# Kernel optimization log

Hardware: AMD Instinct MI355X
Metric: run time of the kernel (lower is better)

Reference implementation:

```python
import jax, jax.numpy as jnp
import numpy as np

B, N, T = 256, 512, 96
E, H, K = 8, 128, 2
PROB_THRESHOLD = 0.05
# SG auto-anneal: first forward sets temperature = t_max = 10.0 (cosine decay at step 0)
TEMP = 10.0


def setup_inputs() -> dict:
    key = jax.random.key(0)
    ks = jax.random.split(key, 8)
    s_g = 1.0 / np.sqrt(T)
    s_1 = 1.0 / np.sqrt(T)
    s_2 = 1.0 / np.sqrt(H)
    return {
        "x": jax.random.normal(ks[0], (B, N, T), dtype=jnp.float32),
        "Wg": jax.random.uniform(ks[1], (E, T), jnp.float32, -s_g, s_g),   # gate Linear(T, E)
        "bg": jax.random.uniform(ks[2], (E,), jnp.float32, -s_g, s_g),
        "W1": jax.random.uniform(ks[3], (E, T, H), jnp.float32, -s_1, s_1),  # stacked MLPExpert fc1
        "b1": jax.random.uniform(ks[4], (E, H), jnp.float32, -s_1, s_1),
        "W2": jax.random.uniform(ks[5], (E, H, T), jnp.float32, -s_2, s_2),  # stacked MLPExpert fc2
        "b2": jax.random.uniform(ks[6], (E, T), jnp.float32, -s_2, s_2),
        "route_scale": jnp.asarray(1.2, dtype=jnp.float32),
    }


def reference(x, Wg, bg, W1, b1, W2, b2, route_scale):
    b, n, t = x.shape
    BN = b * n
    xf = x.reshape(BN, t)                              # [BN, T]

    # ---- SG gate (eval mode: no noise; temp = t_max after first anneal step) ----
    logits = (xf @ Wg.T + bg) / TEMP                   # [BN, E]
    probs = jax.nn.softmax(logits, axis=-1)
    topw, topi = jax.lax.top_k(probs, K)               # [BN, K]
    w = topw / (jnp.sum(topw, axis=-1, keepdims=True) + 1e-12)  # topk_weights_norm

    # ---- SEA routing: capacity generous (never binds for this config); topk indices
    # are distinct so duplicate-expert reroute never triggers. Route is valid iff
    # normalized prob >= prob_threshold; invalid routes are passthrough (copy x). ----
    mask = w >= PROB_THRESHOLD                         # compute_mask [BN, K]

    # ---- SEE experts (MLPExpert with residual), computed densely per expert ----
    h = jax.nn.relu(jnp.einsum('bt,eth->ebh', xf, W1) + b1[:, None, :])   # [E, BN, H]
    y_all = jnp.einsum('ebh,eht->ebt', h, W2) + b2[:, None, :] + xf[None] # [E, BN, T]

    # gather each token's chosen expert outputs
    y_sel = y_all[topi, jnp.arange(BN)[:, None]]       # [BN, K, T]
    contrib = jnp.where(mask[..., None], y_sel, xf[:, None, :])

    # ---- weighted combine (SEE normalizes again, then scales) ----
    wn = w / jnp.clip(jnp.sum(w, axis=-1, keepdims=True), 1e-12)
    mixed = jnp.sum(contrib * wn[..., None], axis=1) * route_scale        # [BN, T]

    util = jnp.sum(mask[..., None] * jax.nn.one_hot(topi, E, dtype=xf.dtype), axis=1)
    return mixed.reshape(b, n, t), util.reshape(b, n, E)
```

## Files before the change

kernel.cpp:

```cpp
#include <hip/hip_runtime.h>
#include <hip/hip_bf16.h>

#define BN_TOTAL   131072
#define T_DIM      96
#define E_NUM      8
#define H_DIM      128
#define CAP        131072
#define PTHRESH    0.05f
#define NBLK       64

typedef _Float16 f16x8 __attribute__((ext_vector_type(8)));
typedef _Float16 f16x4 __attribute__((ext_vector_type(4)));
typedef float    f32x4 __attribute__((ext_vector_type(4)));

#define OFF_TOK    1024
#define OFF_SCALE  (OFF_TOK   + E_NUM * CAP * 4)
#define OFF_MASK   (OFF_SCALE + E_NUM * CAP * 4)
#define OFF_COEF   (OFF_MASK  + BN_TOTAL * 4)
#define OFF_YBUF   (OFF_COEF  + BN_TOTAL * 4)
#define OFF_XH     (OFF_YBUF + 2 * BN_TOTAL * T_DIM * 2)
#define OFF_W1T    (OFF_XH   + BN_TOTAL * T_DIM * 2)
#define OFF_W2T    (OFF_W1T  + E_NUM * H_DIM * T_DIM * 2)
#define WS_NEED    ((size_t)OFF_YBUF + (size_t)2 * BN_TOTAL * T_DIM * 4)


__global__ void zero_cnt_kernel(int* __restrict__ cnt) {
    if (threadIdx.x < E_NUM) cnt[threadIdx.x] = 0;
}

__global__ __launch_bounds__(256) void prep_kernel(
    const float* __restrict__ W1, const float* __restrict__ W2,
    _Float16* __restrict__ w1T, _Float16* __restrict__ w2T,
    int* __restrict__ cnt)
{
    __shared__ _Float16 tile[128 * 136];
    const int tid = threadIdx.x;
    if (blockIdx.x == 0 && tid < E_NUM) cnt[tid] = 0;
    const bool isW1 = blockIdx.x < 8;
    const int e = blockIdx.x & 7;
    const int R = isW1 ? T_DIM : H_DIM;
    const int C = isW1 ? H_DIM : T_DIM;
    const int S = isW1 ? 104 : 136;
    const float* src = (isW1 ? W1 : W2) + (size_t)e * T_DIM * H_DIM;
    _Float16* dst = (isW1 ? w1T : w2T) + (size_t)e * T_DIM * H_DIM;

    const int nb = (R >> 2) * (C >> 2);
    for (int b = tid; b < nb; b += 256) {
        const int r4 = b / (C >> 2), c4 = b % (C >> 2);
#pragma unroll
        for (int i = 0; i < 4; ++i) {
            const float4 v = *reinterpret_cast<const float4*>(src + (size_t)(4 * r4 + i) * C + 4 * c4);
            tile[(4 * c4 + 0) * S + 4 * r4 + i] = (_Float16)v.x;
            tile[(4 * c4 + 1) * S + 4 * r4 + i] = (_Float16)v.y;
            tile[(4 * c4 + 2) * S + 4 * r4 + i] = (_Float16)v.z;
            tile[(4 * c4 + 3) * S + 4 * r4 + i] = (_Float16)v.w;
        }
    }
    __syncthreads();
    const int chunks = C * (R >> 3);
    for (int q = tid; q < chunks; q += 256) {
        const int cr = q / (R >> 3), k = q % (R >> 3);
        *reinterpret_cast<f16x8*>(dst + (size_t)cr * R + 8 * k) =
            *reinterpret_cast<const f16x8*>(&tile[cr * S + 8 * k]);
    }
}

template<bool GATHER>
__global__ __launch_bounds__(1024) void gate_kernel(
    const float* __restrict__ x, const float* __restrict__ Wg,
    const float* __restrict__ bg, const float* __restrict__ rs_p,
    float* __restrict__ mixed, float* __restrict__ util,
    int* __restrict__ cnt, int* __restrict__ toklist, float* __restrict__ scalelist,
    int* __restrict__ maskbuf, float* __restrict__ coefbuf, _Float16* __restrict__ xh)
{
    __shared__ float wg_s[E_NUM][T_DIM];
    __shared__ float bg_s[E_NUM];
    __shared__ int wcnt[16][E_NUM];
    __shared__ int wbase[16][E_NUM];

    const int tid = threadIdx.x;
    for (int i = tid; i < E_NUM * T_DIM; i += 1024) wg_s[i / T_DIM][i % T_DIM] = Wg[i];
    if (tid < E_NUM) bg_s[tid] = bg[tid];
    __syncthreads();

    const int g   = tid >> 2;
    const int sub = tid & 3;
    const int token = blockIdx.x * 256 + g;
    const float* xr_f = x + (size_t)token * T_DIM + sub * 24;

    float4 xv[6];
#pragma unroll
    for (int i = 0; i < 6; ++i) xv[i] = reinterpret_cast<const float4*>(xr_f)[i];

    float logit[E_NUM];
#pragma unroll
    for (int e = 0; e < E_NUM; ++e) logit[e] = 0.0f;
#pragma unroll
    for (int i = 0; i < 6; ++i) {
#pragma unroll
        for (int e = 0; e < E_NUM; ++e) {
            const float4 wv = *reinterpret_cast<const float4*>(&wg_s[e][sub * 24 + 4 * i]);
            logit[e] = fmaf(xv[i].x, wv.x, logit[e]);
            logit[e] = fmaf(xv[i].y, wv.y, logit[e]);
            logit[e] = fmaf(xv[i].z, wv.z, logit[e]);
            logit[e] = fmaf(xv[i].w, wv.w, logit[e]);
        }
    }
#pragma unroll
    for (int e = 0; e < E_NUM; ++e) {
        logit[e] += __shfl_xor(logit[e], 1);
        logit[e] += __shfl_xor(logit[e], 2);
        logit[e] = (logit[e] + bg_s[e]) / 10.0f;
    }

    float mx = logit[0];
#pragma unroll
    for (int e = 1; e < E_NUM; ++e) mx = fmaxf(mx, logit[e]);
    float p[E_NUM]; float s = 0.0f;
#pragma unroll
    for (int e = 0; e < E_NUM; ++e) { p[e] = __expf(logit[e] - mx); s += p[e]; }
    const float inv_s = 1.0f / s;
#pragma unroll
    for (int e = 0; e < E_NUM; ++e) p[e] *= inv_s;

    int i0 = 0; float p0 = p[0];
#pragma unroll
    for (int e = 1; e < E_NUM; ++e) { if (p[e] > p0) { p0 = p[e]; i0 = e; } }
    int i1 = -1; float p1 = -1.0f;
#pragma unroll
    for (int e = 0; e < E_NUM; ++e) { if (e != i0 && p[e] > p1) { p1 = p[e]; i1 = e; } }

    const float denom0 = p0 + p1 + 1e-12f;
    const float w0 = p0 / denom0, w1 = p1 / denom0;
    const bool m0 = (w0 >= PTHRESH), m1 = (w1 >= PTHRESH);
    const float sumw = w0 + w1;
    const float denom1 = fmaxf(sumw, 1e-12f);
    const float wn0 = w0 / denom1, wn1 = w1 / denom1;
    const float rs = *rs_p;
    const float coef = rs * (wn0 + wn1);
    const bool lead = (sub == 0);

    const int lane = tid & 63;
    const int wv_id = tid >> 6;
    const unsigned long long lt = (1ULL << lane) - 1ULL;

    int wcnt_mine = 0, offA = 0, offB = 0;
#pragma unroll
    for (int e = 0; e < E_NUM; ++e) {
        const unsigned long long A = __ballot(lead && m0 && (i0 == e));
        const unsigned long long B = __ballot(lead && m1 && (i1 == e));
        const int na = __popcll(A), nb = __popcll(B);
        if (lane == e) wcnt_mine = na + nb;
        if (lead && m0 && (i0 == e)) offA = __popcll(A & lt);
        if (lead && m1 && (i1 == e)) offB = na + __popcll(B & lt);
    }
    if (lane < E_NUM) wcnt[wv_id][lane] = wcnt_mine;
    __syncthreads();

    int run = 0, c[16];
    if (tid < E_NUM) {
        int tot = 0;
#pragma unroll
        for (int w = 0; w < 16; ++w) { c[w] = wcnt[w][tid]; tot += c[w]; }
        run = atomicAdd(&cnt[tid], tot);
    }

    if (GATHER) {
        _Float16* xr = xh + (size_t)token * T_DIM + sub * 24;
#pragma unroll
        for (int i = 0; i < 6; ++i) {
            f16x4 h4;
            h4[0] = (_Float16)xv[i].x; h4[1] = (_Float16)xv[i].y;
            h4[2] = (_Float16)xv[i].z; h4[3] = (_Float16)xv[i].w;
            reinterpret_cast<f16x4*>(xr)[i] = h4;
        }
        if (lead) { coefbuf[token] = coef; maskbuf[token] = (m0 ? 1 : 0) | (m1 ? 2 : 0); }
    } else {
        float* mr = mixed + (size_t)token * T_DIM + sub * 24;
#pragma unroll
        for (int i = 0; i < 6; ++i)
            reinterpret_cast<float4*>(mr)[i] =
                make_float4(coef * xv[i].x, coef * xv[i].y, coef * xv[i].z, coef * xv[i].w);
    }
    if (lead) {
        float u[E_NUM];
#pragma unroll
        for (int e = 0; e < E_NUM; ++e)
            u[e] = (((e == i0) && m0) || ((e == i1) && m1)) ? 1.0f : 0.0f;
        float4* u4 = reinterpret_cast<float4*>(util + (size_t)token * E_NUM);
        u4[0] = make_float4(u[0], u[1], u[2], u[3]);
        u4[1] = make_float4(u[4], u[5], u[6], u[7]);
    }

    if (tid < E_NUM) {
#pragma unroll
        for (int w = 0; w < 16; ++w) { wbase[w][tid] = run; run += c[w]; }
    }
    __syncthreads();

    if (lead && m0) {
        const int pos = wbase[wv_id][i0] + offA;
        toklist[i0 * CAP + pos] = (token << 1);
        scalelist[i0 * CAP + pos] = rs * wn0;
    }
    if (lead && m1) {
        const int pos = wbase[wv_id][i1] + offB;
        toklist[i1 * CAP + pos] = (token << 1) | 1;
        scalelist[i1 * CAP + pos] = rs * wn1;
    }
}

template<bool GATHER>
__global__ __launch_bounds__(256, 2) void expert_kernel(
    const float* __restrict__ x, const _Float16* __restrict__ xh,
    const float* __restrict__ W1, const float* __restrict__ b1,
    const float* __restrict__ W2, const float* __restrict__ b2,
    const _Float16* __restrict__ w1T, const _Float16* __restrict__ w2T,
    float* __restrict__ mixed, _Float16* __restrict__ ybh,
    const int* __restrict__ cnt, const int* __restrict__ toklist,
    const float* __restrict__ scalelist)
{
    __shared__ __align__(16) _Float16 w1Ls[H_DIM * 104];
    __shared__ __align__(16) _Float16 w2Ls[T_DIM * 136];
    __shared__ __align__(16) _Float16 Hs[64 * 136];

    const int e = blockIdx.y;
    const int count = cnt[e];
    if ((int)blockIdx.x * 64 >= count) return;

    const int tid  = threadIdx.x;
    const int w    = tid >> 6;
    const int lane = tid & 63;
    const int lm   = lane & 15;
    const int lg4  = lane >> 4;
    const int mhalf = w & 1;
    const int nhalf = w >> 1;

    const int*   tl = toklist   + (size_t)e * CAP;
    const float* sl = scalelist + (size_t)e * CAP;

    if (GATHER) {
        const _Float16* w1e = w1T + (size_t)e * H_DIM * T_DIM;
        for (int q = tid; q < 1536; q += 256) {
            const int h = q / 12, cch = q % 12;
            *reinterpret_cast<f16x8*>(&w1Ls[h * 104 + cch * 8]) =
                *reinterpret_cast<const f16x8*>(&w1e[h * T_DIM + cch * 8]);
        }
        const _Float16* w2e = w2T + (size_t)e * H_DIM * T_DIM;
        for (int q = tid; q < 1536; q += 256) {
            const int t = q / 16, cch = q % 16;
            *reinterpret_cast<f16x8*>(&w2Ls[t * 136 + cch * 8]) =
                *reinterpret_cast<const f16x8*>(&w2e[t * H_DIM + cch * 8]);
        }
    } else {
        const float* gW1 = W1 + (size_t)e * T_DIM * H_DIM;
        for (int q = tid; q < H_DIM * T_DIM; q += 256) {
            const int h = q / T_DIM, t = q % T_DIM;
            w1Ls[h * 104 + t] = (_Float16)gW1[(size_t)t * H_DIM + h];
        }
        const float* gW2 = W2 + (size_t)e * H_DIM * T_DIM;
        for (int q = tid; q < H_DIM * T_DIM; q += 256) {
            const int t = q / H_DIM, h = q % H_DIM;
            w2Ls[t * 136 + h] = (_Float16)gW2[(size_t)h * T_DIM + t];
        }
    }
    float4 b1v[4], b2v[3];
#pragma unroll
    for (int n = 0; n < 4; ++n)
        b1v[n] = *reinterpret_cast<const float4*>(b1 + e * H_DIM + nhalf * 64 + n * 16 + lg4 * 4);
#pragma unroll
    for (int n = 0; n < 3; ++n)
        b2v[n] = *reinterpret_cast<const float4*>(b2 + e * T_DIM + nhalf * 48 + n * 16 + lg4 * 4);
    __syncthreads();

    for (int t0 = blockIdx.x * 64; t0 < count; t0 += NBLK * 64) {
        const int nt = min(64, count - t0);

        int packedi[2]; float sci[2]; bool val[2]; int rowi[2];
#pragma unroll
        for (int mt = 0; mt < 2; ++mt) {
            const int slot = (mhalf * 2 + mt) * 16 + lm;
            val[mt] = slot < nt;
            const int gi = t0 + (val[mt] ? slot : 0);
            packedi[mt] = tl[gi];
            rowi[mt] = packedi[mt] >> 1;
            sci[mt] = sl[gi];
        }

        f16x8 xf[2][3];
#pragma unroll
        for (int mt = 0; mt < 2; ++mt)
#pragma unroll
            for (int ks = 0; ks < 3; ++ks) {
                if (GATHER) {
                    xf[mt][ks] = *reinterpret_cast<const f16x8*>(
                        xh + (size_t)rowi[mt] * T_DIM + ks * 32 + lg4 * 8);
                } else {
                    const float* xp = x + (size_t)rowi[mt] * T_DIM + ks * 32 + lg4 * 8;
                    f16x8 v;
#pragma unroll
                    for (int j = 0; j < 8; ++j) v[j] = (_Float16)xp[j];
                    xf[mt][ks] = v;
                }
            }

        f32x4 acc1[2][4];
#pragma unroll
        for (int mt = 0; mt < 2; ++mt)
#pragma unroll
            for (int n = 0; n < 4; ++n) acc1[mt][n] = f32x4{0.f, 0.f, 0.f, 0.f};
#pragma unroll
        for (int ks = 0; ks < 3; ++ks)
#pragma unroll
            for (int n = 0; n < 4; ++n) {
                const f16x8 wa = *reinterpret_cast<const f16x8*>(
                    &w1Ls[(nhalf * 64 + n * 16 + lm) * 104 + ks * 32 + lg4 * 8]);
                acc1[0][n] = __builtin_amdgcn_mfma_f32_16x16x32_f16(wa, xf[0][ks], acc1[0][n], 0, 0, 0);
                acc1[1][n] = __builtin_amdgcn_mfma_f32_16x16x32_f16(wa, xf[1][ks], acc1[1][n], 0, 0, 0);
            }

#pragma unroll
        for (int mt = 0; mt < 2; ++mt) {
            const int tok = (mhalf * 2 + mt) * 16 + lm;
#pragma unroll
            for (int n = 0; n < 4; ++n) {
                const float* bb = reinterpret_cast<const float*>(&b1v[n]);
                f16x4 hv;
#pragma unroll
                for (int r = 0; r < 4; ++r)
                    hv[r] = (_Float16)fmaxf(acc1[mt][n][r] + bb[r], 0.0f);
                *reinterpret_cast<f16x4*>(&Hs[tok * 136 + nhalf * 64 + n * 16 + lg4 * 4]) = hv;
            }
        }
        __syncthreads();

        f32x4 acc2[2][3];
#pragma unroll
        for (int mt = 0; mt < 2; ++mt)
#pragma unroll
            for (int n = 0; n < 3; ++n) acc2[mt][n] = f32x4{0.f, 0.f, 0.f, 0.f};
#pragma unroll
        for (int ks = 0; ks < 4; ++ks) {
            const f16x8 hf0 = *reinterpret_cast<const f16x8*>(
                &Hs[((mhalf * 2 + 0) * 16 + lm) * 136 + ks * 32 + lg4 * 8]);
            const f16x8 hf1 = *reinterpret_cast<const f16x8*>(
                &Hs[((mhalf * 2 + 1) * 16 + lm) * 136 + ks * 32 + lg4 * 8]);
#pragma unroll
            for (int n = 0; n < 3; ++n) {
                const f16x8 wb = *reinterpret_cast<const f16x8*>(
                    &w2Ls[(nhalf * 48 + n * 16 + lm) * 136 + ks * 32 + lg4 * 8]);
                acc2[0][n] = __builtin_amdgcn_mfma_f32_16x16x32_f16(wb, hf0, acc2[0][n], 0, 0, 0);
                acc2[1][n] = __builtin_amdgcn_mfma_f32_16x16x32_f16(wb, hf1, acc2[1][n], 0, 0, 0);
            }
        }
        __syncthreads();

#pragma unroll
        for (int mt = 0; mt < 2; ++mt) {
            if (val[mt]) {
#pragma unroll
                for (int n = 0; n < 3; ++n) {
                    const float* bb = reinterpret_cast<const float*>(&b2v[n]);
                    f16x4 yv;
#pragma unroll
                    for (int r = 0; r < 4; ++r)
                        yv[r] = (_Float16)(sci[mt] * (acc2[mt][n][r] + bb[r]));
                    if (GATHER) {
                        *reinterpret_cast<f16x4*>(
                            ybh + (size_t)packedi[mt] * T_DIM + nhalf * 48 + n * 16 + lg4 * 4) = yv;
                    } else {
#pragma unroll
                        for (int r = 0; r < 4; ++r)
                            atomicAdd(&mixed[(size_t)(packedi[mt] >> 1) * T_DIM +
                                             nhalf * 48 + n * 16 + lg4 * 4 + r], (float)yv[r]);
                    }
                }
            }
        }
    }
}

__global__ __launch_bounds__(256) void finalize_kernel(
    const _Float16* __restrict__ xh, const _Float16* __restrict__ ybh,
    const int* __restrict__ maskbuf, const float* __restrict__ coefbuf,
    float* __restrict__ mixed)
{
    const int tid = threadIdx.x;
    const int token = blockIdx.x * 32 + (tid >> 3);
    const int seg = (tid & 7) * 12;

    const float coef = coefbuf[token];
    const int mask = maskbuf[token];

    const f16x4* xs = reinterpret_cast<const f16x4*>(xh + (size_t)token * T_DIM + seg);
    float4* od = reinterpret_cast<float4*>(mixed + (size_t)token * T_DIM + seg);

    float4 r[3];
#pragma unroll
    for (int q = 0; q < 3; ++q) {
        const f16x4 xv = xs[q];
        r[q] = make_float4(coef * (float)xv[0], coef * (float)xv[1],
                           coef * (float)xv[2], coef * (float)xv[3]);
    }
    if (mask & 1) {
        const f16x4* ys = reinterpret_cast<const f16x4*>(ybh + (size_t)(2 * token) * T_DIM + seg);
#pragma unroll
        for (int q = 0; q < 3; ++q) {
            const f16x4 yv = ys[q];
            r[q].x += (float)yv[0]; r[q].y += (float)yv[1];
            r[q].z += (float)yv[2]; r[q].w += (float)yv[3];
        }
    }
    if (mask & 2) {
        const f16x4* ys = reinterpret_cast<const f16x4*>(ybh + (size_t)(2 * token + 1) * T_DIM + seg);
#pragma unroll
        for (int q = 0; q < 3; ++q) {
            const f16x4 yv = ys[q];
            r[q].x += (float)yv[0]; r[q].y += (float)yv[1];
            r[q].z += (float)yv[2]; r[q].w += (float)yv[3];
        }
    }
#pragma unroll
    for (int q = 0; q < 3; ++q) od[q] = r[q];
}

extern "C" void kernel_launch(void* const* d_in, const int* in_sizes, int n_in,
                              void* d_out, int out_size, void* d_ws, size_t ws_size,
                              hipStream_t stream)
{
    const float* x  = (const float*)d_in[0];
    const float* Wg = (const float*)d_in[1];
    const float* bg = (const float*)d_in[2];
    const float* W1 = (const float*)d_in[3];
    const float* b1 = (const float*)d_in[4];
    const float* W2 = (const float*)d_in[5];
    const float* b2 = (const float*)d_in[6];
    const float* rs = (const float*)d_in[7];

    float* mixed = (float*)d_out;
    float* util  = mixed + (size_t)BN_TOTAL * T_DIM;

    char* ws = (char*)d_ws;
    int*      cnt       = (int*)ws;
    int*      toklist   = (int*)(ws + OFF_TOK);
    float*    scalelist = (float*)(ws + OFF_SCALE);
    int*      maskbuf   = (int*)(ws + OFF_MASK);
    float*    coefbuf   = (float*)(ws + OFF_COEF);
    _Float16* ybh       = (_Float16*)(ws + OFF_YBUF);
    _Float16* xh        = (_Float16*)(ws + OFF_XH);
    _Float16* w1T       = (_Float16*)(ws + OFF_W1T);
    _Float16* w2T       = (_Float16*)(ws + OFF_W2T);

    const bool gather = (ws_size >= WS_NEED);

    if (gather) {
        prep_kernel<<<16, 256, 0, stream>>>(W1, W2, w1T, w2T, cnt);
        gate_kernel<true><<<BN_TOTAL / 256, 1024, 0, stream>>>(
            x, Wg, bg, rs, mixed, util, cnt, toklist, scalelist, maskbuf, coefbuf, xh);
        expert_kernel<true><<<dim3(NBLK, E_NUM), 256, 0, stream>>>(
            x, xh, W1, b1, W2, b2, w1T, w2T, mixed, ybh, cnt, toklist, scalelist);
        finalize_kernel<<<BN_TOTAL / 32, 256, 0, stream>>>(
            xh, ybh, maskbuf, coefbuf, mixed);
    } else {
        zero_cnt_kernel<<<1, 64, 0, stream>>>(cnt);
        gate_kernel<false><<<BN_TOTAL / 256, 1024, 0, stream>>>(
            x, Wg, bg, rs, mixed, util, cnt, toklist, scalelist, maskbuf, coefbuf, xh);
        expert_kernel<false><<<dim3(NBLK, E_NUM), 256, 0, stream>>>(
            x, xh, W1, b1, W2, b2, w1T, w2T, mixed, ybh, cnt, toklist, scalelist);
    }
}
```

Measured before the change: 97.79 us.

## Give each wave its own 16-token slab to drop block-level barriers

The expert kernel's work split changes from a 2x2 token/feature split across the four waves to one where each wave owns 16 tokens and computes all 128 hidden and 96 output features. The hidden activations go to a per-wave LDS slice, so the two __syncthreads per tile are removed. In exchange, each wave reads the whole W1/W2 tile from LDS, so LDS traffic per token doubles, and register pressure rises from the larger accumulator and bias arrays.

```diff
diff --git a/kernel.cpp b/kernel.cpp
--- a/kernel.cpp
+++ b/kernel.cpp
@@ -229,12 +229,10 @@
     if ((int)blockIdx.x * 64 >= count) return;
 
     const int tid  = threadIdx.x;
-    const int w    = tid >> 6;
+    const int wv   = tid >> 6;
     const int lane = tid & 63;
     const int lm   = lane & 15;
     const int lg4  = lane >> 4;
-    const int mhalf = w & 1;
-    const int nhalf = w >> 1;
 
     const int*   tl = toklist   + (size_t)e * CAP;
     const float* sl = scalelist + (size_t)e * CAP;
@@ -264,116 +262,95 @@
             w2Ls[t * 136 + h] = (_Float16)gW2[(size_t)h * T_DIM + t];
         }
     }
-    float4 b1v[4], b2v[3];
-#pragma unroll
-    for (int n = 0; n < 4; ++n)
-        b1v[n] = *reinterpret_cast<const float4*>(b1 + e * H_DIM + nhalf * 64 + n * 16 + lg4 * 4);
-#pragma unroll
-    for (int n = 0; n < 3; ++n)
-        b2v[n] = *reinterpret_cast<const float4*>(b2 + e * T_DIM + nhalf * 48 + n * 16 + lg4 * 4);
+    float4 b1v[8], b2v[6];
+#pragma unroll
+    for (int n = 0; n < 8; ++n)
+        b1v[n] = *reinterpret_cast<const float4*>(b1 + e * H_DIM + n * 16 + lg4 * 4);
+#pragma unroll
+    for (int n = 0; n < 6; ++n)
+        b2v[n] = *reinterpret_cast<const float4*>(b2 + e * T_DIM + n * 16 + lg4 * 4);
     __syncthreads();
+
+    _Float16* HsW = Hs + wv * 16 * 136;
 
     for (int t0 = blockIdx.x * 64; t0 < count; t0 += NBLK * 64) {
         const int nt = min(64, count - t0);
 
-        int packedi[2]; float sci[2]; bool val[2]; int rowi[2];
-#pragma unroll
-        for (int mt = 0; mt < 2; ++mt) {
-            const int slot = (mhalf * 2 + mt) * 16 + lm;
-            val[mt] = slot < nt;
-            const int gi = t0 + (val[mt] ? slot : 0);
-            packedi[mt] = tl[gi];
-            rowi[mt] = packedi[mt] >> 1;
-            sci[mt] = sl[gi];
-        }
-
-        f16x8 xf[2][3];
-#pragma unroll
-        for (int mt = 0; mt < 2; ++mt)
-#pragma unroll
-            for (int ks = 0; ks < 3; ++ks) {
+        const int slot = wv * 16 + lm;
+        const bool valid = slot < nt;
+        const int gi = t0 + (valid ? slot : 0);
+        const int packed = tl[gi];
+        const int row = packed >> 1;
+        const float sc = sl[gi];
+
+        f16x8 xf[3];
+#pragma unroll
+        for (int ks = 0; ks < 3; ++ks) {
+            if (GATHER) {
+                xf[ks] = *reinterpret_cast<const f16x8*>(
+                    xh + (size_t)row * T_DIM + ks * 32 + lg4 * 8);
+            } else {
+                const float* xp = x + (size_t)row * T_DIM + ks * 32 + lg4 * 8;
+                f16x8 v;
+#pragma unroll
+                for (int j = 0; j < 8; ++j) v[j] = (_Float16)xp[j];
+                xf[ks] = v;
+            }
+        }
+
+        f32x4 acc1[8];
+#pragma unroll
+        for (int n = 0; n < 8; ++n) acc1[n] = f32x4{0.f, 0.f, 0.f, 0.f};
+#pragma unroll
+        for (int ks = 0; ks < 3; ++ks)
+#pragma unroll
+            for (int n = 0; n < 8; ++n) {
+                const f16x8 wa = *reinterpret_cast<const f16x8*>(
+                    &w1Ls[(n * 16 + lm) * 104 + ks * 32 + lg4 * 8]);
+                acc1[n] = __builtin_amdgcn_mfma_f32_16x16x32_f16(wa, xf[ks], acc1[n], 0, 0, 0);
+            }
+
+#pragma unroll
+        for (int n = 0; n < 8; ++n) {
+            const float* bb = reinterpret_cast<const float*>(&b1v[n]);
+            f16x4 hv;
+#pragma unroll
+            for (int r = 0; r < 4; ++r)
+                hv[r] = (_Float16)fmaxf(acc1[n][r] + bb[r], 0.0f);
+            *reinterpret_cast<f16x4*>(&HsW[lm * 136 + n * 16 + lg4 * 4]) = hv;
+        }
+
+        f32x4 acc2[6];
+#pragma unroll
+        for (int n = 0; n < 6; ++n) acc2[n] = f32x4{0.f, 0.f, 0.f, 0.f};
+#pragma unroll
+        for (int ks = 0; ks < 4; ++ks) {
+            const f16x8 hf = *reinterpret_cast<const f16x8*>(
+                &HsW[lm * 136 + ks * 32 + lg4 * 8]);
+#pragma unroll
+            for (int n = 0; n < 6; ++n) {
+                const f16x8 wb = *reinterpret_cast<const f16x8*>(
+                    &w2Ls[(n * 16 + lm) * 136 + ks * 32 + lg4 * 8]);
+                acc2[n] = __builtin_amdgcn_mfma_f32_16x16x32_f16(wb, hf, acc2[n], 0, 0, 0);
+            }
+        }
+
+        if (valid) {
+#pragma unroll
+            for (int n = 0; n < 6; ++n) {
+                const float* bb = reinterpret_cast<const float*>(&b2v[n]);
+                f16x4 yv;
+#pragma unroll
+                for (int r = 0; r < 4; ++r)
+                    yv[r] = (_Float16)(sc * (acc2[n][r] + bb[r]));
                 if (GATHER) {
-                    xf[mt][ks] = *reinterpret_cast<const f16x8*>(
-                        xh + (size_t)rowi[mt] * T_DIM + ks * 32 + lg4 * 8);
+                    *reinterpret_cast<f16x4*>(
+                        ybh + (size_t)packed * T_DIM + n * 16 + lg4 * 4) = yv;
                 } else {
-                    const float* xp = x + (size_t)rowi[mt] * T_DIM + ks * 32 + lg4 * 8;
-                    f16x8 v;
-#pragma unroll
-                    for (int j = 0; j < 8; ++j) v[j] = (_Float16)xp[j];
-                    xf[mt][ks] = v;
-                }
-            }
-
-        f32x4 acc1[2][4];
-#pragma unroll
-        for (int mt = 0; mt < 2; ++mt)
-#pragma unroll
-            for (int n = 0; n < 4; ++n) acc1[mt][n] = f32x4{0.f, 0.f, 0.f, 0.f};
-#pragma unroll
-        for (int ks = 0; ks < 3; ++ks)
-#pragma unroll
-            for (int n = 0; n < 4; ++n) {
-                const f16x8 wa = *reinterpret_cast<const f16x8*>(
-                    &w1Ls[(nhalf * 64 + n * 16 + lm) * 104 + ks * 32 + lg4 * 8]);
-                acc1[0][n] = __builtin_amdgcn_mfma_f32_16x16x32_f16(wa, xf[0][ks], acc1[0][n], 0, 0, 0);
-                acc1[1][n] = __builtin_amdgcn_mfma_f32_16x16x32_f16(wa, xf[1][ks], acc1[1][n], 0, 0, 0);
-            }
-
-#pragma unroll
-        for (int mt = 0; mt < 2; ++mt) {
-            const int tok = (mhalf * 2 + mt) * 16 + lm;
-#pragma unroll
-            for (int n = 0; n < 4; ++n) {
-                const float* bb = reinterpret_cast<const float*>(&b1v[n]);
-                f16x4 hv;
-#pragma unroll
-                for (int r = 0; r < 4; ++r)
-                    hv[r] = (_Float16)fmaxf(acc1[mt][n][r] + bb[r], 0.0f);
-                *reinterpret_cast<f16x4*>(&Hs[tok * 136 + nhalf * 64 + n * 16 + lg4 * 4]) = hv;
-            }
-        }
-        __syncthreads();
-
-        f32x4 acc2[2][3];
-#pragma unroll
-        for (int mt = 0; mt < 2; ++mt)
-#pragma unroll
-            for (int n = 0; n < 3; ++n) acc2[mt][n] = f32x4{0.f, 0.f, 0.f, 0.f};
-#pragma unroll
-        for (int ks = 0; ks < 4; ++ks) {
-            const f16x8 hf0 = *reinterpret_cast<const f16x8*>(
-                &Hs[((mhalf * 2 + 0) * 16 + lm) * 136 + ks * 32 + lg4 * 8]);
-            const f16x8 hf1 = *reinterpret_cast<const f16x8*>(
-                &Hs[((mhalf * 2 + 1) * 16 + lm) * 136 + ks * 32 + lg4 * 8]);
-#pragma unroll
-            for (int n = 0; n < 3; ++n) {
-                const f16x8 wb = *reinterpret_cast<const f16x8*>(
-                    &w2Ls[(nhalf * 48 + n * 16 + lm) * 136 + ks * 32 + lg4 * 8]);
-                acc2[0][n] = __builtin_amdgcn_mfma_f32_16x16x32_f16(wb, hf0, acc2[0][n], 0, 0, 0);
-                acc2[1][n] = __builtin_amdgcn_mfma_f32_16x16x32_f16(wb, hf1, acc2[1][n], 0, 0, 0);
-            }
-        }
-        __syncthreads();
-
-#pragma unroll
-        for (int mt = 0; mt < 2; ++mt) {
-            if (val[mt]) {
-#pragma unroll
-                for (int n = 0; n < 3; ++n) {
-                    const float* bb = reinterpret_cast<const float*>(&b2v[n]);
-                    f16x4 yv;
 #pragma unroll
                     for (int r = 0; r < 4; ++r)
-                        yv[r] = (_Float16)(sci[mt] * (acc2[mt][n][r] + bb[r]));
-                    if (GATHER) {
-                        *reinterpret_cast<f16x4*>(
-                            ybh + (size_t)packedi[mt] * T_DIM + nhalf * 48 + n * 16 + lg4 * 4) = yv;
-                    } else {
-#pragma unroll
-                        for (int r = 0; r < 4; ++r)
-                            atomicAdd(&mixed[(size_t)(packedi[mt] >> 1) * T_DIM +
-                                             nhalf * 48 + n * 16 + lg4 * 4 + r], (float)yv[r]);
-                    }
+                        atomicAdd(&mixed[(size_t)(packed >> 1) * T_DIM +
+                                         n * 16 + lg4 * 4 + r], (float)yv[r]);
                 }
             }
         }
```

Result: slower. 120.9 us (+23.7%).
